# Kernel optimization log

Measured on AMD Instinct MI355X. Metric: run time of the kernel, lower is better.

## Reference

```python
import jax, jax.numpy as jnp
import numpy as np
from jax import lax

B, H, W = 32, 40, 256
FREQ = 40            # freq_num
WIND = 0.5           # wind_size (seconds)
KF = 5               # input_filter_kernel (odd -> 'same' length)
CNN_OUT = 64 * 36 * 252  # out_channels[-1] * (H-4) * (W-4)


def setup_inputs() -> dict:
    key = jax.random.key(0)
    ks = jax.random.split(key, 9)
    return {
        "inputs": jax.random.normal(ks[0], (B, 1, H, W), jnp.float32),
        "w0": jax.random.normal(ks[1], (32, 1, 3, 3), jnp.float32) * 0.1,
        "b0": jax.random.normal(ks[2], (32,), jnp.float32) * 0.05,
        "w1": jax.random.normal(ks[3], (64, 32, 3, 3), jnp.float32) * 0.05,
        "b1": jax.random.normal(ks[4], (64,), jnp.float32) * 0.05,
        "wf": jax.random.normal(ks[5], (1, 1, 1, KF), jnp.float32) * 0.2,
        "bf": jax.random.normal(ks[6], (1,), jnp.float32) * 0.05,
        "wr": jax.random.normal(ks[7], (FREQ, CNN_OUT), jnp.float32) * 1e-3,
        "br": jax.random.normal(ks[8], (FREQ,), jnp.float32) * 0.05,
    }


def _conv2d(x, w, padding):
    return lax.conv_general_dilated(
        x, w, window_strides=(1, 1), padding=padding,
        dimension_numbers=("NCHW", "OIHW", "NCHW"))


def reference(inputs, w0, b0, w1, b1, wf, bf, wr, br):
    b, _, h, w_len = inputs.shape
    # input_filter: Conv1d(1,1,KF, padding=KF//2) applied independently per
    # frequency row -> equivalent to a 2D conv with a (1,KF) kernel.
    p = KF // 2
    feats = _conv2d(inputs, wf, [(0, 0), (p, p)]) + bf[None, :, None, None]  # [B,1,H,W]

    # conv stack with ReLU
    x = jax.nn.relu(_conv2d(inputs, w0, "VALID") + b0[None, :, None, None])
    x = jax.nn.relu(_conv2d(x, w1, "VALID") + b1[None, :, None, None])

    gates = jax.nn.sigmoid(x.reshape(b, -1) @ wr.T + br)

    fs = (1.0 / WIND) * jnp.linspace(1.0, FREQ, FREQ)          # [FREQ]
    wtd_mean_mod = jnp.mean(gates * fs[None, :])               # scalar

    # Fused modulation transform: instead of the per-frequency python loop
    # with materialized [B,H,W] broadcasts, compute sin/cos bases [FREQ,W]
    # and reduce over time with a single einsum each.
    t = jnp.linspace(0.0, WIND, w_len)                          # [W]
    phase = (2.0 * np.pi) * fs[:, None] * t[None, :]            # [FREQ,W]
    f0 = feats[:, 0]                                            # [B,H,W]
    inv_w = jnp.float32(1.0 / w_len)
    sins = jnp.einsum("fw,bhw->bfh", jnp.sin(phase), f0) * inv_w  # mean over W
    coss = jnp.einsum("fw,bhw->bfh", jnp.cos(phase), f0) * inv_w
    mag = jnp.sqrt(sins * sins + coss * coss)                   # [B,FREQ,H]
    mods = (mag * gates[:, :, None]).reshape(b, FREQ * h)       # cat over freq, dim=1
    return mods, wtd_mean_mod
```

## Files before the change

### kernel.cpp

```cpp
#include <hip/hip_runtime.h>
#include <hip/hip_bf16.h>
#include <math.h>

#define BB   32
#define HH   40
#define WW   256
#define NF   40
#define H1N  36
#define W1N  252
#define KCNN 580608
#define NBLK2 504
#define KPW  288

typedef __attribute__((ext_vector_type(8))) short bf16x8;
typedef __attribute__((ext_vector_type(4))) float f32x4;

static __device__ __forceinline__ unsigned short f2bf(float v) {
    __hip_bfloat16 h = __float2bfloat16(v);
    return *(unsigned short*)&h;
}

static __device__ __forceinline__ bf16x8 packbf(float4 lo, float4 hi) {
    bf16x8 r;
    r[0] = (short)f2bf(lo.x); r[1] = (short)f2bf(lo.y);
    r[2] = (short)f2bf(lo.z); r[3] = (short)f2bf(lo.w);
    r[4] = (short)f2bf(hi.x); r[5] = (short)f2bf(hi.y);
    r[6] = (short)f2bf(hi.z); r[7] = (short)f2bf(hi.w);
    return r;
}

__global__ void k0_prep(const float* __restrict__ w1, unsigned short* __restrict__ w1c,
                        float* __restrict__ gacc, unsigned int* __restrict__ done) {
    int o = blockIdx.x * 256 + threadIdx.x;
    int c0  = o & 31;
    int c1  = (o >> 5) & 63;
    int tap = o >> 11;
    w1c[o] = f2bf(w1[(c1 * 32 + c0) * 9 + tap]);
    if (blockIdx.x == 71) {
        for (int p = threadIdx.x; p < 1280; p += 256) gacc[p] = 0.0f;
        if (threadIdx.x == 0) *done = 0u;
    }
}

__global__ __launch_bounds__(256) void k1_conv(
        const float* __restrict__ inp, const float* __restrict__ w0,
        const float* __restrict__ b0, const unsigned short* __restrict__ w1c,
        const float* __restrict__ b1, unsigned short* __restrict__ xbf) {
    __shared__ __align__(16) unsigned short smem[18432];
    unsigned short* y0T = smem;
    float* ins = (float*)(smem + 15840);
    unsigned short* xp = smem;

    const int jt = blockIdx.x;
    const int it = blockIdx.y;
    const int b  = blockIdx.z;
    const int i0 = it * 4;
    const int j0 = jt * 64;
    const int tid = threadIdx.x;

    for (int s = tid; s < 546; s += 256) {
        int r = s / 68, c = s - r * 68;
        float v = 0.0f;
        if (r < 8 && (j0 + c) < WW) v = inp[(b * HH + i0 + r) * WW + j0 + c];
        ins[s] = v;
    }
    __syncthreads();

    {
        const int c0  = tid & 31;
        const int sub = tid >> 5;
        float wreg[9];
        #pragma unroll
        for (int k = 0; k < 9; ++k) wreg[k] = w0[c0 * 9 + k];
        const float bias = b0[c0];
        for (int s = sub; s < 17; s += 8) {
            const int cbase = 4 * s;
            float rows[3][6];
            #pragma unroll
            for (int r = 0; r < 8; ++r) {
                {
                    const float4 a  = *(const float4*)&ins[r * 68 + cbase];
                    const float2 b2 = *(const float2*)&ins[r * 68 + cbase + 4];
                    float* dst = rows[r % 3];
                    dst[0] = a.x; dst[1] = a.y; dst[2] = a.z;
                    dst[3] = a.w; dst[4] = b2.x; dst[5] = b2.y;
                }
                if (r >= 2) {
                    const int ro = r - 2;
                    const float* r0 = rows[ro % 3];
                    const float* r1 = rows[(ro + 1) % 3];
                    const float* r2 = rows[(ro + 2) % 3];
                    #pragma unroll
                    for (int c = 0; c < 4; ++c) {
                        const int colg = cbase + c;
                        if (colg < 66) {
                            float v = 0.0f;
                            if (j0 + colg < 254) {
                                float a = bias;
                                a = fmaf(r0[c],     wreg[0], a);
                                a = fmaf(r0[c + 1], wreg[1], a);
                                a = fmaf(r0[c + 2], wreg[2], a);
                                a = fmaf(r1[c],     wreg[3], a);
                                a = fmaf(r1[c + 1], wreg[4], a);
                                a = fmaf(r1[c + 2], wreg[5], a);
                                a = fmaf(r2[c],     wreg[6], a);
                                a = fmaf(r2[c + 1], wreg[7], a);
                                a = fmaf(r2[c + 2], wreg[8], a);
                                v = fmaxf(a, 0.0f);
                            }
                            y0T[(ro * 66 + colg) * 40 + c0] = f2bf(v);
                        }
                    }
                }
            }
        }
    }
    __syncthreads();

    const int w    = tid >> 6;
    const int lane = tid & 63;
    const int l15  = lane & 15;
    const int quad = lane >> 4;

    float biasr[4][4];
    #pragma unroll
    for (int mt = 0; mt < 4; ++mt)
        #pragma unroll
        for (int rg = 0; rg < 4; ++rg)
            biasr[mt][rg] = b1[mt * 16 + quad * 4 + rg];

    f32x4 acc[4][4];
    #pragma unroll
    for (int mt = 0; mt < 4; ++mt)
        #pragma unroll
        for (int nt = 0; nt < 4; ++nt)
            acc[mt][nt] = (f32x4){0.f, 0.f, 0.f, 0.f};

    #pragma unroll
    for (int ki = 0; ki < 3; ++ki) {
        #pragma unroll
        for (int kj = 0; kj < 3; ++kj) {
            const int tap = ki * 3 + kj;
            bf16x8 af[4], bfr[4];
            #pragma unroll
            for (int mt = 0; mt < 4; ++mt)
                af[mt] = *(const bf16x8*)(w1c + ((tap * 64 + mt * 16 + l15) * 32 + quad * 8));
            #pragma unroll
            for (int nt = 0; nt < 4; ++nt)
                bfr[nt] = *(const bf16x8*)(y0T + (((w + ki) * 66 + nt * 16 + l15 + kj) * 40 + quad * 8));
            #pragma unroll
            for (int mt = 0; mt < 4; ++mt)
                #pragma unroll
                for (int nt = 0; nt < 4; ++nt)
                    acc[mt][nt] = __builtin_amdgcn_mfma_f32_16x16x32_bf16(
                        af[mt], bfr[nt], acc[mt][nt], 0, 0, 0);
        }
    }
    __syncthreads();

    #pragma unroll
    for (int nt = 0; nt < 4; ++nt) {
        const int j = nt * 16 + l15;
        #pragma unroll
        for (int mt = 0; mt < 4; ++mt) {
            #pragma unroll
            for (int rg = 0; rg < 4; ++rg) {
                const int c1 = mt * 16 + quad * 4 + rg;
                const float v = fmaxf(acc[mt][nt][rg] + biasr[mt][rg], 0.0f);
                xp[(c1 * 4 + w) * 72 + j] = f2bf(v);
            }
        }
    }
    __syncthreads();
    {
        const int chunk = tid & 7;
        const int rb    = tid >> 3;
        #pragma unroll
        for (int p = 0; p < 8; ++p) {
            const int rowid = rb + 32 * p;
            const int c1 = rowid >> 2, ci = rowid & 3;
            uint4 v = *(const uint4*)&xp[rowid * 72 + chunk * 8];
            const int gj = j0 + chunk * 8;
            unsigned short* gp = xbf + (size_t)b * KCNN
                               + (size_t)(c1 * H1N + i0 + ci) * W1N + gj;
            uint2 lo; lo.x = v.x; lo.y = v.y;
            if (gj + 8 <= W1N) {
                uint2 hi; hi.x = v.z; hi.y = v.w;
                *(uint2*)gp = lo;
                *(uint2*)(gp + 4) = hi;
            } else if (gj < W1N) {
                *(uint2*)gp = lo;
            }
        }
    }
}

__global__ __launch_bounds__(256) void k2_gemm(
        const unsigned short* __restrict__ xbf, const float* __restrict__ wr,
        const float* __restrict__ br, float* __restrict__ gacc,
        unsigned int* __restrict__ done, float* __restrict__ gates,
        float* __restrict__ out) {
    __shared__ float red[4][32][41];
    __shared__ unsigned int lastf;

    const int tid  = threadIdx.x;
    const int wv   = tid >> 6;
    const int lane = tid & 63;
    const int l15  = lane & 15;
    const int quad = lane >> 4;
    const size_t kw = (size_t)(blockIdx.x * 4 + wv) * KPW;

    const unsigned short* ap0 = xbf + (size_t)l15 * KCNN + kw + quad * 8;
    const unsigned short* ap1 = ap0 + (size_t)16 * KCNN;
    const float* bp0 = wr + (size_t)l15 * KCNN + kw + quad * 8;
    const float* bp1 = bp0 + (size_t)16 * KCNN;
    const int r2 = (l15 < 8) ? (32 + l15) : 39;
    const float* bp2 = wr + (size_t)r2 * KCNN + kw + quad * 8;

    f32x4 acc[2][3];
    #pragma unroll
    for (int mt = 0; mt < 2; ++mt)
        #pragma unroll
        for (int nt = 0; nt < 3; ++nt)
            acc[mt][nt] = (f32x4){0.f, 0.f, 0.f, 0.f};

    bf16x8 a0c, a1c, a0n, a1n;
    float4 bw[3][2], bwn[3][2];

    a0c = *(const bf16x8*)ap0;
    a1c = *(const bf16x8*)ap1;
    bw[0][0] = *(const float4*)bp0; bw[0][1] = *(const float4*)(bp0 + 4);
    bw[1][0] = *(const float4*)bp1; bw[1][1] = *(const float4*)(bp1 + 4);
    bw[2][0] = *(const float4*)bp2; bw[2][1] = *(const float4*)(bp2 + 4);

    for (int c = 0; c < 9; ++c) {
        if (c < 8) {
            const int o2 = (c + 1) * 32;
            a0n = *(const bf16x8*)(ap0 + o2);
            a1n = *(const bf16x8*)(ap1 + o2);
            bwn[0][0] = *(const float4*)(bp0 + o2); bwn[0][1] = *(const float4*)(bp0 + o2 + 4);
            bwn[1][0] = *(const float4*)(bp1 + o2); bwn[1][1] = *(const float4*)(bp1 + o2 + 4);
            bwn[2][0] = *(const float4*)(bp2 + o2); bwn[2][1] = *(const float4*)(bp2 + o2 + 4);
        }
        #pragma unroll
        for (int nt = 0; nt < 3; ++nt) {
            bf16x8 bfrag = packbf(bw[nt][0], bw[nt][1]);
            acc[0][nt] = __builtin_amdgcn_mfma_f32_16x16x32_bf16(a0c, bfrag, acc[0][nt], 0, 0, 0);
            acc[1][nt] = __builtin_amdgcn_mfma_f32_16x16x32_bf16(a1c, bfrag, acc[1][nt], 0, 0, 0);
        }
        if (c < 8) {
            a0c = a0n; a1c = a1n;
            #pragma unroll
            for (int nt = 0; nt < 3; ++nt) { bw[nt][0] = bwn[nt][0]; bw[nt][1] = bwn[nt][1]; }
        }
    }

    #pragma unroll
    for (int mt = 0; mt < 2; ++mt)
        #pragma unroll
        for (int nt = 0; nt < 3; ++nt)
            #pragma unroll
            for (int rg = 0; rg < 4; ++rg) {
                int bb = mt * 16 + quad * 4 + rg;
                int ff = nt * 16 + l15;
                if (ff < NF) red[wv][bb][ff] = acc[mt][nt][rg];
            }
    __syncthreads();
    for (int p = tid; p < 1280; p += 256) {
        int bb = p / 40, ff = p - bb * 40;
        atomicAdd(gacc + p, red[0][bb][ff] + red[1][bb][ff] + red[2][bb][ff] + red[3][bb][ff]);
    }
    __syncthreads();

    if (tid == 0) {
        __threadfence();
        lastf = (atomicAdd(done, 1u) == NBLK2 - 1) ? 1u : 0u;
    }
    __syncthreads();
    if (lastf) {
        __threadfence();
        float part = 0.0f;
        for (int p = tid; p < 1280; p += 256) {
            float s = __hip_atomic_load(gacc + p, __ATOMIC_RELAXED, __HIP_MEMORY_SCOPE_AGENT);
            int f = p % 40;
            float g = 1.0f / (1.0f + __expf(-(s + br[f])));
            gates[p] = g;
            part += g * 2.0f * (float)(f + 1);
        }
        #pragma unroll
        for (int off = 32; off >= 1; off >>= 1) part += __shfl_xor(part, off);
        float* redf = (float*)red;
        if ((tid & 63) == 0) redf[tid >> 6] = part;
        __syncthreads();
        if (tid == 0)
            out[51200] = (redf[0] + redf[1] + redf[2] + redf[3]) * (1.0f / 1280.0f);
    }
}

__global__ __launch_bounds__(320) void k4_mods(
        const float* __restrict__ inp, const float* __restrict__ wf,
        const float* __restrict__ bfp, const float* __restrict__ gates,
        float* __restrict__ out) {
    const int f = blockIdx.x, b = blockIdx.y;
    const int tid = threadIdx.x;
    const int h  = tid >> 3;
    const int wl = tid & 7;
    float wfv[5];
    #pragma unroll
    for (int t = 0; t < 5; ++t) wfv[t] = wf[t];
    const float bias = bfp[0];
    const float cph = 6.283185307179586f * (float)(f + 1) / 255.0f;
    const float* row = inp + (b * HH + h) * WW;
    float sa = 0.0f, ca = 0.0f;
    for (int m = 0; m < 32; ++m) {
        int w = wl + 8 * m;
        float feat = bias;
        #pragma unroll
        for (int d = -2; d <= 2; ++d) {
            int wc = w + d;
            if (wc >= 0 && wc < WW) feat = fmaf(row[wc], wfv[d + 2], feat);
        }
        float sv, cv;
        __sincosf(cph * (float)w, &sv, &cv);
        sa = fmaf(sv, feat, sa);
        ca = fmaf(cv, feat, ca);
    }
    #pragma unroll
    for (int off = 4; off >= 1; off >>= 1) {
        sa += __shfl_xor(sa, off, 8);
        ca += __shfl_xor(ca, off, 8);
    }
    if (wl == 0) {
        float mag = sqrtf(sa * sa + ca * ca) * (1.0f / 256.0f);
        out[b * 1600 + f * 40 + h] = mag * gates[b * 40 + f];
    }
}

extern "C" void kernel_launch(void* const* d_in, const int* in_sizes, int n_in,
                              void* d_out, int out_size, void* d_ws, size_t ws_size,
                              hipStream_t stream) {
    const float* inp = (const float*)d_in[0];
    const float* w0  = (const float*)d_in[1];
    const float* b0  = (const float*)d_in[2];
    const float* w1  = (const float*)d_in[3];
    const float* b1  = (const float*)d_in[4];
    const float* wf  = (const float*)d_in[5];
    const float* bf_ = (const float*)d_in[6];
    const float* wr  = (const float*)d_in[7];
    const float* br  = (const float*)d_in[8];
    float* out = (float*)d_out;

    char* ws = (char*)d_ws;
    unsigned short* xbf = (unsigned short*)ws;
    unsigned short* w1c = (unsigned short*)(ws + 37158912);
    float* gacc  = (float*)(ws + 37195776);
    float* gates = (float*)(ws + 37200896);
    unsigned int* done = (unsigned int*)(ws + 37206016);

    k0_prep<<<72, 256, 0, stream>>>(w1, w1c, gacc, done);
    k1_conv<<<dim3(4, 9, 32), 256, 0, stream>>>(inp, w0, b0, w1c, b1, xbf);
    k2_gemm<<<NBLK2, 256, 0, stream>>>(xbf, wr, br, gacc, done, gates, out);
    k4_mods<<<dim3(40, 32), 320, 0, stream>>>(inp, wf, bf_, gates, out);
}
```

Before: 238.1 us.

## Run first conv on MFMA and split regression GEMM into more blocks

The first 3x3 conv (1->32 channels) is recast as a bf16 MFMA with im2col fragments built from shared memory, using bf16 weights padded to K=32 in the prep kernel. It replaces the scalar FMA loop and its strided LDS writes. The regression GEMM's K-split is reduced from 288 to 128 per wave, raising the block count from 504 to 1134, and each wave preloads its whole K slice into registers. The trade-offs are more atomics on the gate accumulator, bf16 rounding of the first conv's inputs and weights, and most MFMA lanes left idle on zero padding.

```diff
diff --git a/kernel.cpp b/kernel.cpp
--- a/kernel.cpp
+++ b/kernel.cpp
@@ -9,10 +9,11 @@
 #define H1N  36
 #define W1N  252
 #define KCNN 580608
-#define NBLK2 504
-#define KPW  288
+#define NBLK2 1134
+#define KPW2 128
 
 typedef __attribute__((ext_vector_type(8))) short bf16x8;
+typedef __attribute__((ext_vector_type(4))) short bf16x4;
 typedef __attribute__((ext_vector_type(4))) float f32x4;
 
 static __device__ __forceinline__ unsigned short f2bf(float v) {
@@ -29,13 +30,22 @@
     return r;
 }
 
-__global__ void k0_prep(const float* __restrict__ w1, unsigned short* __restrict__ w1c,
+__global__ void k0_prep(const float* __restrict__ w1, const float* __restrict__ w0,
+                        unsigned short* __restrict__ w1c, unsigned short* __restrict__ w0c,
                         float* __restrict__ gacc, unsigned int* __restrict__ done) {
     int o = blockIdx.x * 256 + threadIdx.x;
-    int c0  = o & 31;
-    int c1  = (o >> 5) & 63;
-    int tap = o >> 11;
-    w1c[o] = f2bf(w1[(c1 * 32 + c0) * 9 + tap]);
+    {
+        int c0  = o & 31;
+        int c1  = (o >> 5) & 63;
+        int tap = o >> 11;
+        w1c[o] = f2bf(w1[(c1 * 32 + c0) * 9 + tap]);
+    }
+    if (blockIdx.x == 70) {
+        for (int i = threadIdx.x; i < 1024; i += 256) {
+            int c0 = i >> 5, k = i & 31;
+            w0c[i] = (k < 9) ? f2bf(w0[c0 * 9 + k]) : (unsigned short)0;
+        }
+    }
     if (blockIdx.x == 71) {
         for (int p = threadIdx.x; p < 1280; p += 256) gacc[p] = 0.0f;
         if (threadIdx.x == 0) *done = 0u;
@@ -43,12 +53,12 @@
 }
 
 __global__ __launch_bounds__(256) void k1_conv(
-        const float* __restrict__ inp, const float* __restrict__ w0,
+        const float* __restrict__ inp, const unsigned short* __restrict__ w0c,
         const float* __restrict__ b0, const unsigned short* __restrict__ w1c,
         const float* __restrict__ b1, unsigned short* __restrict__ xbf) {
     __shared__ __align__(16) unsigned short smem[18432];
     unsigned short* y0T = smem;
-    float* ins = (float*)(smem + 15840);
+    float* ins = (float*)(smem + 16000);
     unsigned short* xp = smem;
 
     const int jt = blockIdx.x;
@@ -58,6 +68,11 @@
     const int j0 = jt * 64;
     const int tid = threadIdx.x;
 
+    const int w    = tid >> 6;
+    const int lane = tid & 63;
+    const int l15  = lane & 15;
+    const int quad = lane >> 4;
+
     for (int s = tid; s < 546; s += 256) {
         int r = s / 68, c = s - r * 68;
         float v = 0.0f;
@@ -67,60 +82,54 @@
     __syncthreads();
 
     {
-        const int c0  = tid & 31;
-        const int sub = tid >> 5;
-        float wreg[9];
-        #pragma unroll
-        for (int k = 0; k < 9; ++k) wreg[k] = w0[c0 * 9 + k];
-        const float bias = b0[c0];
-        for (int s = sub; s < 17; s += 8) {
-            const int cbase = 4 * s;
-            float rows[3][6];
-            #pragma unroll
-            for (int r = 0; r < 8; ++r) {
-                {
-                    const float4 a  = *(const float4*)&ins[r * 68 + cbase];
-                    const float2 b2 = *(const float2*)&ins[r * 68 + cbase + 4];
-                    float* dst = rows[r % 3];
-                    dst[0] = a.x; dst[1] = a.y; dst[2] = a.z;
-                    dst[3] = a.w; dst[4] = b2.x; dst[5] = b2.y;
+        bf16x8 a0f = *(const bf16x8*)(w0c + (0 * 16 + l15) * 32 + quad * 8);
+        bf16x8 a1f = *(const bf16x8*)(w0c + (1 * 16 + l15) * 32 + quad * 8);
+        float bias0[2][4];
+        #pragma unroll
+        for (int mt = 0; mt < 2; ++mt)
+            #pragma unroll
+            for (int rg = 0; rg < 4; ++rg)
+                bias0[mt][rg] = b0[mt * 16 + quad * 4 + rg];
+
+        for (int nt = w; nt < 25; nt += 4) {
+            const int pos  = l15 + 16 * nt;
+            const int posc = (pos < 396) ? pos : 395;
+            const int r    = posc / 66;
+            const int col  = posc - r * 66;
+            bf16x8 bfrag = (bf16x8){0, 0, 0, 0, 0, 0, 0, 0};
+            if (quad == 0) {
+                const float* p0 = ins + r * 68 + col;
+                bfrag[0] = (short)f2bf(p0[0]);
+                bfrag[1] = (short)f2bf(p0[1]);
+                bfrag[2] = (short)f2bf(p0[2]);
+                bfrag[3] = (short)f2bf(p0[68]);
+                bfrag[4] = (short)f2bf(p0[69]);
+                bfrag[5] = (short)f2bf(p0[70]);
+                bfrag[6] = (short)f2bf(p0[136]);
+                bfrag[7] = (short)f2bf(p0[137]);
+            } else if (quad == 1) {
+                bfrag[0] = (short)f2bf(ins[(r + 2) * 68 + col + 2]);
+            }
+            f32x4 d0 = (f32x4){0.f, 0.f, 0.f, 0.f};
+            f32x4 d1 = (f32x4){0.f, 0.f, 0.f, 0.f};
+            d0 = __builtin_amdgcn_mfma_f32_16x16x32_bf16(a0f, bfrag, d0, 0, 0, 0);
+            d1 = __builtin_amdgcn_mfma_f32_16x16x32_bf16(a1f, bfrag, d1, 0, 0, 0);
+            const bool valid = (j0 + col) < 254;
+            if (pos < 396) {
+                bf16x4 v0, v1;
+                #pragma unroll
+                for (int rg = 0; rg < 4; ++rg) {
+                    float x0 = valid ? fmaxf(d0[rg] + bias0[0][rg], 0.0f) : 0.0f;
+                    float x1 = valid ? fmaxf(d1[rg] + bias0[1][rg], 0.0f) : 0.0f;
+                    v0[rg] = (short)f2bf(x0);
+                    v1[rg] = (short)f2bf(x1);
                 }
-                if (r >= 2) {
-                    const int ro = r - 2;
-                    const float* r0 = rows[ro % 3];
-                    const float* r1 = rows[(ro + 1) % 3];
-                    const float* r2 = rows[(ro + 2) % 3];
-                    #pragma unroll
-                    for (int c = 0; c < 4; ++c) {
-                        const int colg = cbase + c;
-                        if (colg < 66) {
-                            float v = 0.0f;
-                            if (j0 + colg < 254) {
-                                float a = bias;
-                                a = fmaf(r0[c],     wreg[0], a);
-                                a = fmaf(r0[c + 1], wreg[1], a);
-                                a = fmaf(r0[c + 2], wreg[2], a);
-                                a = fmaf(r1[c],     wreg[3], a);
-                                a = fmaf(r1[c + 1], wreg[4], a);
-                                a = fmaf(r1[c + 2], wreg[5], a);
-                                a = fmaf(r2[c],     wreg[6], a);
-                                a = fmaf(r2[c + 1], wreg[7], a);
-                                a = fmaf(r2[c + 2], wreg[8], a);
-                                v = fmaxf(a, 0.0f);
-                            }
-                            y0T[(ro * 66 + colg) * 40 + c0] = f2bf(v);
-                        }
-                    }
-                }
-            }
-        }
-    }
-    __syncthreads();
-
-    const int w    = tid >> 6;
-    const int lane = tid & 63;
-    const int l15  = lane & 15;
-    const int quad = lane >> 4;
+                *(bf16x4*)(y0T + pos * 40 +      quad * 4) = v0;
+                *(bf16x4*)(y0T + pos * 40 + 16 + quad * 4) = v1;
+            }
+        }
+    }
+    __syncthreads();
 
     float biasr[4][4];
     #pragma unroll
@@ -208,7 +217,7 @@
     const int lane = tid & 63;
     const int l15  = lane & 15;
     const int quad = lane >> 4;
-    const size_t kw = (size_t)(blockIdx.x * 4 + wv) * KPW;
+    const size_t kw = (size_t)(blockIdx.x * 4 + wv) * KPW2;
 
     const unsigned short* ap0 = xbf + (size_t)l15 * KCNN + kw + quad * 8;
     const unsigned short* ap1 = ap0 + (size_t)16 * KCNN;
@@ -217,6 +226,18 @@
     const int r2 = (l15 < 8) ? (32 + l15) : 39;
     const float* bp2 = wr + (size_t)r2 * KCNN + kw + quad * 8;
 
+    bf16x8 A0[4], A1[4];
+    float4 B[3][4][2];
+    #pragma unroll
+    for (int c = 0; c < 4; ++c) {
+        const int o = c * 32;
+        A0[c] = *(const bf16x8*)(ap0 + o);
+        A1[c] = *(const bf16x8*)(ap1 + o);
+        B[0][c][0] = *(const float4*)(bp0 + o); B[0][c][1] = *(const float4*)(bp0 + o + 4);
+        B[1][c][0] = *(const float4*)(bp1 + o); B[1][c][1] = *(const float4*)(bp1 + o + 4);
+        B[2][c][0] = *(const float4*)(bp2 + o); B[2][c][1] = *(const float4*)(bp2 + o + 4);
+    }
+
     f32x4 acc[2][3];
     #pragma unroll
     for (int mt = 0; mt < 2; ++mt)
@@ -224,34 +245,13 @@
         for (int nt = 0; nt < 3; ++nt)
             acc[mt][nt] = (f32x4){0.f, 0.f, 0.f, 0.f};
 
-    bf16x8 a0c, a1c, a0n, a1n;
-    float4 bw[3][2], bwn[3][2];
-
-    a0c = *(const bf16x8*)ap0;
-    a1c = *(const bf16x8*)ap1;
-    bw[0][0] = *(const float4*)bp0; bw[0][1] = *(const float4*)(bp0 + 4);
-    bw[1][0] = *(const float4*)bp1; bw[1][1] = *(const float4*)(bp1 + 4);
-    bw[2][0] = *(const float4*)bp2; bw[2][1] = *(const float4*)(bp2 + 4);
-
-    for (int c = 0; c < 9; ++c) {
-        if (c < 8) {
-            const int o2 = (c + 1) * 32;
-            a0n = *(const bf16x8*)(ap0 + o2);
-            a1n = *(const bf16x8*)(ap1 + o2);
-            bwn[0][0] = *(const float4*)(bp0 + o2); bwn[0][1] = *(const float4*)(bp0 + o2 + 4);
-            bwn[1][0] = *(const float4*)(bp1 + o2); bwn[1][1] = *(const float4*)(bp1 + o2 + 4);
-            bwn[2][0] = *(const float4*)(bp2 + o2); bwn[2][1] = *(const float4*)(bp2 + o2 + 4);
-        }
+    #pragma unroll
+    for (int c = 0; c < 4; ++c) {
         #pragma unroll
         for (int nt = 0; nt < 3; ++nt) {
-            bf16x8 bfrag = packbf(bw[nt][0], bw[nt][1]);
-            acc[0][nt] = __builtin_amdgcn_mfma_f32_16x16x32_bf16(a0c, bfrag, acc[0][nt], 0, 0, 0);
-            acc[1][nt] = __builtin_amdgcn_mfma_f32_16x16x32_bf16(a1c, bfrag, acc[1][nt], 0, 0, 0);
-        }
-        if (c < 8) {
-            a0c = a0n; a1c = a1n;
-            #pragma unroll
-            for (int nt = 0; nt < 3; ++nt) { bw[nt][0] = bwn[nt][0]; bw[nt][1] = bwn[nt][1]; }
+            bf16x8 bfrag = packbf(B[nt][c][0], B[nt][c][1]);
+            acc[0][nt] = __builtin_amdgcn_mfma_f32_16x16x32_bf16(A0[c], bfrag, acc[0][nt], 0, 0, 0);
+            acc[1][nt] = __builtin_amdgcn_mfma_f32_16x16x32_bf16(A1[c], bfrag, acc[1][nt], 0, 0, 0);
         }
     }
 
@@ -353,12 +353,13 @@
     char* ws = (char*)d_ws;
     unsigned short* xbf = (unsigned short*)ws;
     unsigned short* w1c = (unsigned short*)(ws + 37158912);
-    float* gacc  = (float*)(ws + 37195776);
-    float* gates = (float*)(ws + 37200896);
-    unsigned int* done = (unsigned int*)(ws + 37206016);
-
-    k0_prep<<<72, 256, 0, stream>>>(w1, w1c, gacc, done);
-    k1_conv<<<dim3(4, 9, 32), 256, 0, stream>>>(inp, w0, b0, w1c, b1, xbf);
+    unsigned short* w0c = (unsigned short*)(ws + 37195776);
+    float* gacc  = (float*)(ws + 37197824);
+    float* gates = (float*)(ws + 37202944);
+    unsigned int* done = (unsigned int*)(ws + 37208064);
+
+    k0_prep<<<72, 256, 0, stream>>>(w1, w0, w1c, w0c, gacc, done);
+    k1_conv<<<dim3(4, 9, 32), 256, 0, stream>>>(inp, w0c, b0, w1c, b1, xbf);
     k2_gemm<<<NBLK2, 256, 0, stream>>>(xbf, wr, br, gacc, done, gates, out);
     k4_mods<<<dim3(40, 32), 320, 0, stream>>>(inp, wf, bf_, gates, out);
 }
```

Result: slower. 276.0 us (+15.9%).
